# Performance work log

Measured on AMD Instinct MI355X. Metric: run time of the kernel, lower is better.

Reference implementation:

```python
import jax, jax.numpy as jnp
import numpy as np

WEMD, TAGSET, TEMD, RANK = 400, 50, 20, 396
SEQ, BATCH = 512, 32


def setup_inputs() -> dict:
    key = jax.random.key(0)
    ks = jax.random.split(key, 7)
    std = 0.1545
    return {
        "word_emd": jax.random.normal(ks[0], (SEQ, BATCH, WEMD), dtype=jnp.float32),
        "tag_emd": jax.random.normal(ks[1], (TAGSET, TEMD), dtype=jnp.float32) * std,
        "T": jax.random.normal(ks[2], (WEMD, RANK), dtype=jnp.float32) * std,
        "U": jax.random.normal(ks[3], (WEMD, RANK), dtype=jnp.float32) * std,
        "V": jax.random.normal(ks[4], (TEMD, RANK), dtype=jnp.float32) * std,
        "W": jax.random.normal(ks[5], (TEMD, RANK), dtype=jnp.float32) * std,
        "first_wemb": jax.random.normal(ks[6], (1, WEMD), dtype=jnp.float32) * std,
    }


def reference(word_emd, tag_emd, T, U, V, W, first_wemb):
    # neighbor == 'prev': shift word embeddings right by one along seq,
    # prepending the learned first_wemb broadcast over batch.
    seq, batch, wemd = word_emd.shape
    first = jnp.broadcast_to(first_wemb.reshape(1, 1, wemd), (1, batch, wemd))
    neighbor_word_emd = jnp.concatenate([first, word_emd[:-1]], axis=0)  # [n,a,w]

    g0 = jnp.matmul(word_emd, U)          # [n,a,k]
    g1 = jnp.matmul(neighbor_word_emd, T) # [n,a,k]
    g2 = jnp.matmul(tag_emd, V)           # [b,k]
    g3 = jnp.matmul(tag_emd, W)           # [c,k]

    # Fused quadrilinear contraction: avoids materializing [n,a,b,k]
    # (same math as einsum('nak,bk->nabk') then 'nabk,ck->nabc').
    score = jnp.einsum('nak,bk,ck->nabc', g0 * g1, g2, g3)
    return score
```

## Files before the change

### kernel.cpp

```cpp
#include <hip/hip_runtime.h>

typedef unsigned short u16;
typedef __bf16 bf16x8 __attribute__((ext_vector_type(8)));
typedef float f32x4 __attribute__((ext_vector_type(4)));

#define WEMD 400
#define RANK 396
#define NA   16384
#define KP   416
#define K2   448
#define BSTR 896
#define NBC  2500
#define NBCP 2560

#define OFF_WBF  0u
#define OFF_UBT  13658112u
#define OFF_TBT  14084096u
#define OFF_G    14689280u
#define OFF_H    16983040u

__device__ __forceinline__ u16 f2bf(float f) {
  union { float f; unsigned u; } v; v.f = f;
  unsigned u = v.u;
  return (u16)((u + 0x7FFFu + ((u >> 16) & 1u)) >> 16);
}

typedef __attribute__((address_space(3))) unsigned char lds_byte;
typedef __attribute__((address_space(1))) const unsigned char glob_byte;

__device__ __forceinline__ void gload16(const void* g, void* l) {
  __builtin_amdgcn_global_load_lds((glob_byte*)g, (lds_byte*)l, 16, 0, 0);
}

__global__ __launch_bounds__(256) void prep_all(
    const float* __restrict__ word, const float* __restrict__ first,
    const float* __restrict__ U, const float* __restrict__ T,
    const float* __restrict__ tag, const float* __restrict__ V,
    const float* __restrict__ W,
    u16* __restrict__ Wbf, u16* __restrict__ Ubt, u16* __restrict__ Tbt,
    u16* __restrict__ G) {
  const int R0 = 16416 * 104;
  const int R1 = 416 << 9;
  const int R2 = NBCP * K2;
  const int total = R0 + R1 + R2;
  for (int i = blockIdx.x * 256 + threadIdx.x; i < total; i += gridDim.x * 256) {
    if (i < R0) {
      int r = i / 104, c4 = i - r * 104;
      ushort4 o = {0, 0, 0, 0};
      if (c4 < 100) {
        const float* src = (r < 32) ? (first + c4 * 4)
                                    : (word + (size_t)(r - 32) * WEMD + c4 * 4);
        float4 v = *(const float4*)src;
        o.x = f2bf(v.x); o.y = f2bf(v.y); o.z = f2bf(v.z); o.w = f2bf(v.w);
      }
      *(ushort4*)(Wbf + (size_t)r * KP + c4 * 4) = o;
    } else if (i < R0 + R1) {
      int j = i - R0;
      int n = j & 511, k = j >> 9;
      u16 uo = 0, to = 0;
      if (n < RANK && k < WEMD) {
        uo = f2bf(U[(size_t)k * RANK + n]);
        to = f2bf(T[(size_t)k * RANK + n]);
      }
      Ubt[(size_t)n * KP + k] = uo;
      Tbt[(size_t)n * KP + k] = to;
    } else {
      int j = i - R0 - R1;
      int bc = j / K2, k = j - bc * K2;
      u16 g = 0;
      if (bc < NBC && k < RANK) {
        int b = bc / 50, c = bc - b * 50;
        float a2 = 0.f, a3 = 0.f;
        #pragma unroll
        for (int e = 0; e < 20; ++e) {
          a2 += tag[b * 20 + e] * V[e * RANK + k];
          a3 += tag[c * 20 + e] * W[e * RANK + k];
        }
        g = f2bf(a2 * a3);
      }
      G[(size_t)bc * K2 + k] = g;
    }
  }
}

__global__ __launch_bounds__(256) void gemm_h(const u16* __restrict__ Wbf,
                                              const u16* __restrict__ Ubt,
                                              const u16* __restrict__ Tbt,
                                              u16* __restrict__ H) {
  __shared__ u16 As0[128 * 32], As1[128 * 32], Bu[128 * 32], Bt[128 * 32];
  const int tid = threadIdx.x;
  const int l = tid & 63, w = tid >> 6;
  const int wm = w >> 1, wn = w & 1;
  const int tm = (blockIdx.x >> 2) * 128, tn = (blockIdx.x & 3) * 128;

  f32x4 acc0[4][4] = {}, acc1[4][4] = {};

  const int srow = tid >> 2;
  const int scolb = (tid & 3) * 16;
  const char* gA0 = (const char*)Wbf + (size_t)(tm + 32 + srow) * 832 + scolb;
  const char* gA1 = (const char*)Wbf + (size_t)(tm + srow) * 832 + scolb;
  const char* gU  = (const char*)Ubt + (size_t)(tn + srow) * 832 + scolb;
  const char* gT  = (const char*)Tbt + (size_t)(tn + srow) * 832 + scolb;
  char* lA0 = (char*)As0 + tid * 16;
  char* lA1 = (char*)As1 + tid * 16;
  char* lU  = (char*)Bu  + tid * 16;
  char* lT  = (char*)Bt  + tid * 16;

  const int fo_a = (wm * 64 + (l & 15)) * 32 + (l >> 4) * 8;
  const int fo_b = (wn * 64 + (l & 15)) * 32 + (l >> 4) * 8;

  for (int kt = 0; kt < 13; ++kt) {
    const int kb = kt * 64;
    gload16(gA0 + kb, lA0); gload16(gA0 + kb + (size_t)64 * 832, lA0 + 4096);
    gload16(gA1 + kb, lA1); gload16(gA1 + kb + (size_t)64 * 832, lA1 + 4096);
    gload16(gU  + kb, lU ); gload16(gU  + kb + (size_t)64 * 832, lU  + 4096);
    gload16(gT  + kb, lT ); gload16(gT  + kb + (size_t)64 * 832, lT  + 4096);
    __syncthreads();
    bf16x8 a0[4], a1[4], bu[4], bt[4];
    #pragma unroll
    for (int i = 0; i < 4; ++i) {
      a0[i] = *(const bf16x8*)(As0 + fo_a + i * 16 * 32);
      a1[i] = *(const bf16x8*)(As1 + fo_a + i * 16 * 32);
      bu[i] = *(const bf16x8*)(Bu  + fo_b + i * 16 * 32);
      bt[i] = *(const bf16x8*)(Bt  + fo_b + i * 16 * 32);
    }
    #pragma unroll
    for (int i = 0; i < 4; ++i)
      #pragma unroll
      for (int j = 0; j < 4; ++j) {
        acc0[i][j] = __builtin_amdgcn_mfma_f32_16x16x32_bf16(a0[i], bu[j], acc0[i][j], 0, 0, 0);
        acc1[i][j] = __builtin_amdgcn_mfma_f32_16x16x32_bf16(a1[i], bt[j], acc1[i][j], 0, 0, 0);
      }
    __syncthreads();
  }

  const int r4 = (l >> 4) * 4, cc = l & 15;
  #pragma unroll
  for (int i = 0; i < 4; ++i)
    #pragma unroll
    for (int j = 0; j < 4; ++j) {
      const int col = tn + wn * 64 + j * 16 + cc;
      if (col < K2) {
        #pragma unroll
        for (int r = 0; r < 4; ++r) {
          const int rowg = tm + wm * 64 + i * 16 + r4 + r;
          H[(size_t)rowg * K2 + col] = f2bf(acc0[i][j][r] * acc1[i][j][r]);
        }
      }
    }
}

__global__ __launch_bounds__(256, 3) void gemm_big2(const u16* __restrict__ H,
                                                    const u16* __restrict__ G,
                                                    float* __restrict__ out) {
  __shared__ u16 lds[2 * 8192];
  char* ldsb = (char*)lds;
  const int tid = threadIdx.x;
  const int lane = tid & 63, wid = tid >> 6;
  const int wm = wid >> 1, wn = wid & 1;

  int bs = (int)blockIdx.x;
  bs = (bs & 7) * 320 + (bs >> 3);
  const int tm = (bs / 20) * 128, tn = (bs % 20) * 128;

  const char* gH = (const char*)H + (size_t)tm * BSTR;
  const char* gG = (const char*)G + (size_t)tn * BSTR;

  int sP[4], sR[4], sC[4];
  #pragma unroll
  for (int q = 0; q < 4; ++q) {
    int P = tid * 16 + q * 4096;
    int L = P ^ (((P >> 7) & 7) << 4);
    sP[q] = P; sR[q] = L >> 7; sC[q] = L & 127;
  }
  const int arow = (lane & 15) * 128;
  const int sw = (lane & 7) << 4;

  f32x4 acc[4][4] = {};

  for (int kt = 0; kt < 7; ++kt) {
    const int kb = kt * 128;
    #pragma unroll
    for (int q = 0; q < 4; ++q) {
      gload16(gH + (size_t)sR[q] * BSTR + kb + sC[q], ldsb + sP[q]);
      gload16(gG + (size_t)sR[q] * BSTR + kb + sC[q], ldsb + 16384 + sP[q]);
    }
    __syncthreads();
    #pragma unroll
    for (int ks = 0; ks < 2; ++ks) {
      const int csw = (ks * 64 + (lane >> 4) * 16) ^ sw;
      bf16x8 a[4], b[4];
      #pragma unroll
      for (int rf = 0; rf < 4; ++rf)
        a[rf] = *(const bf16x8*)(ldsb + wm * 8192 + rf * 2048 + arow + csw);
      #pragma unroll
      for (int cf = 0; cf < 4; ++cf)
        b[cf] = *(const bf16x8*)(ldsb + 16384 + wn * 8192 + cf * 2048 + arow + csw);
      #pragma unroll
      for (int rf = 0; rf < 4; ++rf)
        #pragma unroll
        for (int cf = 0; cf < 4; ++cf)
          acc[rf][cf] = __builtin_amdgcn_mfma_f32_16x16x32_bf16(a[rf], b[cf], acc[rf][cf], 0, 0, 0);
    }
    __syncthreads();
  }

  const int r4 = (lane >> 4) * 4, cc = lane & 15;
  const int rbase = tm + wm * 64 + r4;
  const int cbase = tn + wn * 64 + cc;
  #pragma unroll
  for (int rf = 0; rf < 4; ++rf)
    #pragma unroll
    for (int cf = 0; cf < 4; ++cf) {
      const int col = cbase + cf * 16;
      if (col < NBC) {
        #pragma unroll
        for (int rr = 0; rr < 4; ++rr)
          out[(size_t)(rbase + rf * 16 + rr) * NBC + col] = acc[rf][cf][rr];
      }
    }
}

extern "C" void kernel_launch(void* const* d_in, const int* in_sizes, int n_in,
                              void* d_out, int out_size, void* d_ws, size_t ws_size,
                              hipStream_t stream) {
  const float* word  = (const float*)d_in[0];
  const float* tag   = (const float*)d_in[1];
  const float* Tm    = (const float*)d_in[2];
  const float* Um    = (const float*)d_in[3];
  const float* Vm    = (const float*)d_in[4];
  const float* Wm    = (const float*)d_in[5];
  const float* first = (const float*)d_in[6];
  float* out = (float*)d_out;
  char* ws = (char*)d_ws;

  u16*   Wbf = (u16*)(ws + OFF_WBF);
  u16*   Ubt = (u16*)(ws + OFF_UBT);
  u16*   Tbt = (u16*)(ws + OFF_TBT);
  u16*   G   = (u16*)(ws + OFF_G);
  u16*   H   = (u16*)(ws + OFF_H);

  hipLaunchKernelGGL(prep_all, dim3(2048), dim3(256), 0, stream,
                     word, first, Um, Tm, tag, Vm, Wm, Wbf, Ubt, Tbt, G);
  hipLaunchKernelGGL(gemm_h,   dim3(128 * 4), dim3(256), 0, stream, Wbf, Ubt, Tbt, H);
  hipLaunchKernelGGL(gemm_big2, dim3(2560), dim3(256), 0, stream, H, G, out);
}
```

Before: 115.6 us.

## Triple-buffer LDS in big GEMM with vmcnt-based prefetch pipeline

```diff
diff --git a/kernel.cpp b/kernel.cpp
--- a/kernel.cpp
+++ b/kernel.cpp
@@ -31,6 +31,11 @@
 __device__ __forceinline__ void gload16(const void* g, void* l) {
   __builtin_amdgcn_global_load_lds((glob_byte*)g, (lds_byte*)l, 16, 0, 0);
 }
+
+#define FENCE() asm volatile("" ::: "memory")
+#define BARRIER() do { FENCE(); __builtin_amdgcn_s_barrier(); FENCE(); } while (0)
+#define VMCNT0() asm volatile("s_waitcnt vmcnt(0)" ::: "memory")
+#define VMCNT4() asm volatile("s_waitcnt vmcnt(4)" ::: "memory")
 
 __global__ __launch_bounds__(256) void prep_all(
     const float* __restrict__ word, const float* __restrict__ first,
@@ -150,10 +155,10 @@
     }
 }
 
-__global__ __launch_bounds__(256, 3) void gemm_big2(const u16* __restrict__ H,
+__global__ __launch_bounds__(256, 3) void gemm_big4(const u16* __restrict__ H,
                                                     const u16* __restrict__ G,
                                                     float* __restrict__ out) {
-  __shared__ u16 lds[2 * 8192];
+  __shared__ u16 lds[3 * 8192];
   char* ldsb = (char*)lds;
   const int tid = threadIdx.x;
   const int lane = tid & 63, wid = tid >> 6;
@@ -163,47 +168,64 @@
   bs = (bs & 7) * 320 + (bs >> 3);
   const int tm = (bs / 20) * 128, tn = (bs % 20) * 128;
 
-  const char* gH = (const char*)H + (size_t)tm * BSTR;
-  const char* gG = (const char*)G + (size_t)tn * BSTR;
-
-  int sP[4], sR[4], sC[4];
-  #pragma unroll
-  for (int q = 0; q < 4; ++q) {
+  const char* gHb = (const char*)H;
+  const char* gGb = (const char*)G;
+
+  int aP[2], bP[2];
+  long aOff[2], bOff[2];
+  #pragma unroll
+  for (int q = 0; q < 2; ++q) {
     int P = tid * 16 + q * 4096;
-    int L = P ^ (((P >> 7) & 7) << 4);
-    sP[q] = P; sR[q] = L >> 7; sC[q] = L & 127;
-  }
-  const int arow = (lane & 15) * 128;
-  const int sw = (lane & 7) << 4;
+    int row = P >> 6;
+    int lcol = (P & 63) ^ (((row >> 1) & 3) << 4);
+    aP[q] = P;        aOff[q] = (long)(tm + row) * BSTR + lcol;
+    bP[q] = 8192 + P; bOff[q] = (long)(tn + row) * BSTR + lcol;
+  }
+
+  int aro[4], bro[4];
+  #pragma unroll
+  for (int f = 0; f < 4; ++f) {
+    int ra = wm * 64 + f * 16 + (lane & 15);
+    int rb = wn * 64 + f * 16 + (lane & 15);
+    aro[f] = ra * 64 + (((lane >> 4) * 16) ^ (((ra >> 1) & 3) << 4));
+    bro[f] = rb * 64 + (((lane >> 4) * 16) ^ (((rb >> 1) & 3) << 4));
+  }
 
   f32x4 acc[4][4] = {};
 
-  for (int kt = 0; kt < 7; ++kt) {
-    const int kb = kt * 128;
-    #pragma unroll
-    for (int q = 0; q < 4; ++q) {
-      gload16(gH + (size_t)sR[q] * BSTR + kb + sC[q], ldsb + sP[q]);
-      gload16(gG + (size_t)sR[q] * BSTR + kb + sC[q], ldsb + 16384 + sP[q]);
-    }
-    __syncthreads();
-    #pragma unroll
-    for (int ks = 0; ks < 2; ++ks) {
-      const int csw = (ks * 64 + (lane >> 4) * 16) ^ sw;
-      bf16x8 a[4], b[4];
-      #pragma unroll
-      for (int rf = 0; rf < 4; ++rf)
-        a[rf] = *(const bf16x8*)(ldsb + wm * 8192 + rf * 2048 + arow + csw);
+#define ISSUEQ(j)                                                        \
+  do {                                                                   \
+    char* _r = ldsb + ((j) % 3) * 16384;                                 \
+    const int _kb = (j) * 64;                                            \
+    _Pragma("unroll")                                                    \
+    for (int q = 0; q < 2; ++q) {                                        \
+      gload16(gHb + aOff[q] + _kb, _r + aP[q]);                          \
+      gload16(gGb + bOff[q] + _kb, _r + bP[q]);                          \
+    }                                                                    \
+  } while (0)
+
+  ISSUEQ(0); ISSUEQ(1);
+
+  for (int j = 0; j < 14; ++j) {
+    if (j < 13) { VMCNT4(); }
+    else        { VMCNT0(); }
+    BARRIER();
+    if (j + 2 < 14) ISSUEQ(j + 2);
+
+    char* reg = ldsb + (j % 3) * 16384;
+    bf16x8 a[4], b[4];
+    #pragma unroll
+    for (int f = 0; f < 4; ++f) {
+      a[f] = *(const bf16x8*)(reg + aro[f]);
+      b[f] = *(const bf16x8*)(reg + 8192 + bro[f]);
+    }
+    #pragma unroll
+    for (int rf = 0; rf < 4; ++rf)
       #pragma unroll
       for (int cf = 0; cf < 4; ++cf)
-        b[cf] = *(const bf16x8*)(ldsb + 16384 + wn * 8192 + cf * 2048 + arow + csw);
-      #pragma unroll
-      for (int rf = 0; rf < 4; ++rf)
-        #pragma unroll
-        for (int cf = 0; cf < 4; ++cf)
-          acc[rf][cf] = __builtin_amdgcn_mfma_f32_16x16x32_bf16(a[rf], b[cf], acc[rf][cf], 0, 0, 0);
-    }
-    __syncthreads();
-  }
+        acc[rf][cf] = __builtin_amdgcn_mfma_f32_16x16x32_bf16(a[rf], b[cf], acc[rf][cf], 0, 0, 0);
+  }
+#undef ISSUEQ
 
   const int r4 = (lane >> 4) * 4, cc = lane & 15;
   const int rbase = tm + wm * 64 + r4;
@@ -243,5 +265,5 @@
   hipLaunchKernelGGL(prep_all, dim3(2048), dim3(256), 0, stream,
                      word, first, Um, Tm, tag, Vm, Wm, Wbf, Ubt, Tbt, G);
   hipLaunchKernelGGL(gemm_h,   dim3(128 * 4), dim3(256), 0, stream, Wbf, Ubt, Tbt, H);
-  hipLaunchKernelGGL(gemm_big2, dim3(2560), dim3(256), 0, stream, H, G, out);
-}
+  hipLaunchKernelGGL(gemm_big4, dim3(2560), dim3(256), 0, stream, H, G, out);
+}
```

After: 123.0 us. 6.5% more time.
